# Performance work log

Hardware: AMD Instinct MI355X
Metric: run time of the kernel (lower is better)

## Reference

```python
import jax, jax.numpy as jnp
import numpy as np

N, E, D, H, C = 50000, 250000, 300, 4, 75  # nodes, edges, in_size=300, heads=4, out=75 (H*C=300)


def setup_inputs() -> dict:
    key = jax.random.key(0)
    ks = jax.random.split(key, 32)
    rn = lambda k, shape, s=0.05: jax.random.normal(k, shape, jnp.float32) * s
    inp = {}
    inp['x'] = rn(ks[0], (N, D), 1.0)
    inp['edge_index'] = jax.random.randint(ks[1], (2, E), 0, N, dtype=jnp.int32)
    inp['edge_attr'] = rn(ks[2], (E, 4), 1.0)
    inp['obj_normals'] = rn(ks[3], (N, 3), 1.0)
    # parameters (Linear stored as [in, out] so y = x @ W + b)
    inp['Wq'] = rn(ks[4], (D, H * C)); inp['bq'] = rn(ks[5], (H * C,))
    inp['Wk'] = rn(ks[6], (D, H * C)); inp['bk'] = rn(ks[7], (H * C,))
    inp['Wv'] = rn(ks[8], (D, H * C)); inp['bv'] = rn(ks[9], (H * C,))
    inp['We'] = rn(ks[10], (D, H * C))               # lin_edge, no bias
    inp['Wn'] = rn(ks[11], (3, D)); inp['bn'] = rn(ks[12], (D,))      # map_normal
    inp['Wxy'] = rn(ks[13], (2, D)); inp['bxy'] = rn(ks[14], (D,))    # map_xy_relative_coord
    inp['Wloc'] = rn(ks[15], (3 * D, D)); inp['bloc'] = rn(ks[16], (D,))  # map_back_edge_loc
    inp['Wobj'] = rn(ks[17], (2 * D, D)); inp['bobj'] = rn(ks[18], (D,))  # map_back_edge_obj
    inp['Wfus'] = rn(ks[19], (2 * D, D)); inp['bfus'] = rn(ks[20], (D,))  # hv_words_fusion
    inp['Wcls'] = rn(ks[21], (D, 5)); inp['bcls'] = rn(ks[22], (5,))      # horizontal_word_cls
    inp['Wskip'] = rn(ks[23], (D, H * C)); inp['bskip'] = rn(ks[24], (H * C,))  # lin_skip
    inp['vocab'] = rn(ks[25], (7, D), 1.0)  # spatial_vocab_we
    return inp


def reference(x, edge_index, edge_attr, obj_normals,
              Wq, bq, Wk, bk, Wv, bv, We, Wn, bn, Wxy, bxy,
              Wloc, bloc, Wobj, bobj, Wfus, bfus, Wcls, bcls,
              Wskip, bskip, vocab):
    src, dst = edge_index[0], edge_index[1]  # x_j = x[src], x_i = x[dst]
    x_i = x[dst]
    x_j = x[src]
    q = (x_i @ Wq + bq).reshape(E, H, C)
    k = (x_j @ Wk + bk).reshape(E, H, C)
    # vertical (top/bottom) word embeddings gated by edge_attr signs
    top = (edge_attr[:, 0] > 0).astype(x.dtype)[:, None] * vocab[0][None, :]
    bot = (edge_attr[:, 1] < 0).astype(x.dtype)[:, None] * vocab[1][None, :]
    vert = top + bot                                           # [E, D]
    # horizontal word probabilities from geometry + feature cues
    ni = obj_normals[dst] @ Wn + bn
    nj = obj_normals[src] @ Wn + bn
    xy = edge_attr[:, 2:4] @ Wxy + bxy
    loc = jnp.concatenate([xy, ni, nj], axis=1) @ Wloc + bloc
    obj = jnp.concatenate([x_i, x_j - x_i], axis=1) @ Wobj + bobj
    prob = jax.nn.softmax(jnp.tanh(obj + loc) @ Wcls + bcls, axis=1)   # [E, 5]
    horiz = prob @ vocab[2:7]                                  # [E, D]
    edge_word = jnp.concatenate([vert, horiz], axis=1) @ Wfus + bfus   # [E, D]
    ef = (edge_word @ We).reshape(E, H, C)                     # lin_edge
    k = k + ef
    # scaled dot-product attention with per-destination-node softmax
    alpha = (q * k).sum(-1) / jnp.asarray(np.sqrt(C), x.dtype)  # [E, H]
    m = jax.ops.segment_max(alpha, dst, num_segments=N)
    alpha = jnp.exp(alpha - m[dst])
    den = jax.ops.segment_sum(alpha, dst, num_segments=N)
    alpha = alpha / den[dst]
    v = (x_j @ Wv + bv).reshape(E, H, C) + ef
    msg = v * alpha[..., None]                                  # [E, H, C]
    out = jax.ops.segment_sum(msg, dst, num_segments=N).reshape(N, H * C)
    out = out + x @ Wskip + bskip                               # concat heads + root skip
    return out
```

## Files before the change

### kernel.cpp

```cpp
#include <hip/hip_runtime.h>
#include <hip/hip_bf16.h>
#include <math.h>

#define NDIM 300
#define KPAD 320
#define NREAL 1800
#define NPAD 1920

typedef __hip_bfloat16 bf16;
typedef __attribute__((ext_vector_type(8))) short short8;
typedef __attribute__((ext_vector_type(4))) float f32x4;

__device__ __forceinline__ void gl_lds16(const void* g, void* l) {
    __builtin_amdgcn_global_load_lds(
        (const __attribute__((address_space(1))) void*)g,
        (__attribute__((address_space(3))) void*)l, 16, 0, 0);
}

__device__ __forceinline__ float bflo(uint u) { return __uint_as_float(u << 16); }
__device__ __forceinline__ float bfhi(uint u) { return __uint_as_float(u & 0xFFFF0000u); }

__global__ void small_pre(
    const float* __restrict__ Wn, const float* __restrict__ bn,
    const float* __restrict__ Wxy, const float* __restrict__ bxy,
    const float* __restrict__ Wloc, const float* __restrict__ bloc,
    const float* __restrict__ bobj,
    const float* __restrict__ Wfus,
    const float* __restrict__ vocab,
    float* __restrict__ Wn1, float* __restrict__ Wn2,
    float* __restrict__ Mxy, float* __restrict__ bgeo,
    float* __restrict__ vf5, float* __restrict__ t0, float* __restrict__ t1)
{
    int i = blockIdx.x * blockDim.x + threadIdx.x;
    if (i < 900) {
        int r = i / 300, c = i % 300;
        float s = 0.f;
        for (int k = 0; k < 300; k++) s += Wn[r*300+k] * Wloc[(300+k)*300+c];
        Wn1[i] = s;
    } else if (i < 1800) {
        int j = i - 900; int r = j/300, c = j%300;
        float s = 0.f;
        for (int k = 0; k < 300; k++) s += Wn[r*300+k] * Wloc[(600+k)*300+c];
        Wn2[j] = s;
    } else if (i < 2400) {
        int j = i - 1800; int r = j/300, c = j%300;
        float s = 0.f;
        for (int k = 0; k < 300; k++) s += Wxy[r*300+k] * Wloc[k*300+c];
        Mxy[j] = 2.f * s;
    } else if (i < 2700) {
        int c = i - 2400;
        float s = bloc[c] + bobj[c];
        for (int k = 0; k < 300; k++) s += bxy[k] * Wloc[k*300+c];
        for (int k = 0; k < 300; k++) s += bn[k] * (Wloc[(300+k)*300+c] + Wloc[(600+k)*300+c]);
        bgeo[c] = 2.f * s;
    } else if (i < 4200) {
        int j = i - 2700; int p = j/300, c = j%300;
        float s = 0.f;
        for (int k = 0; k < 300; k++) s += vocab[(2+p)*300+k] * Wfus[(300+k)*300+c];
        vf5[j] = s;
    } else if (i < 4500) {
        int c = i - 4200;
        float s = 0.f;
        for (int k = 0; k < 300; k++) s += vocab[k] * Wfus[k*300+c];
        t0[c] = s;
    } else if (i < 4800) {
        int c = i - 4500;
        float s = 0.f;
        for (int k = 0; k < 300; k++) s += vocab[300+k] * Wfus[k*300+c];
        t1[c] = s;
    }
}

__global__ void small_pre2(
    const float* __restrict__ We, const float* __restrict__ bfus,
    const float* __restrict__ vf5, const float* __restrict__ t0, const float* __restrict__ t1,
    const float* __restrict__ Wcls,
    float* __restrict__ E8, float* __restrict__ WclsT)
{
    int i = blockIdx.x * blockDim.x + threadIdx.x;
    if (i < 2400) {
        int r = i / 300, c = i % 300;
        const float* src;
        if (r == 0) src = t0;
        else if (r == 1) src = t1;
        else if (r == 7) src = bfus;
        else src = vf5 + (r - 2) * 300;
        float s = 0.f;
        for (int k = 0; k < 300; k++) s += src[k] * We[k*300+c];
        E8[i] = s;
    } else if (i < 3900) {
        int j = i - 2400; int cl = j / 300, c = j % 300;
        WclsT[cl * 300 + c] = Wcls[c * 5 + cl];
    }
}

__global__ void pack_w(
    const float* __restrict__ Wq, const float* __restrict__ Wk,
    const float* __restrict__ Wv, const float* __restrict__ Wskip,
    const float* __restrict__ Wobj,
    const float* __restrict__ Wn1, const float* __restrict__ Wn2,
    const float* __restrict__ bq, const float* __restrict__ bk,
    const float* __restrict__ bv, const float* __restrict__ bskip,
    bf16* __restrict__ WcatT, float* __restrict__ bcat)
{
    int i = blockIdx.x * blockDim.x + threadIdx.x;
    if (i < NREAL) {
        int c = i;
        float b = 0.f;
        if (c < 600)       { if (!(c & 1)) b = bq[c >> 1]; }
        else if (c < 1200) { int cc = c - 600; if (cc & 1) b = bk[cc >> 1]; }
        else if (c < 1500) b = bv[c - 1200];
        else               b = bskip[c - 1500];
        bcat[i] = b;
    }
    if (i < NPAD * KPAD) {
        int cp = i / KPAD, k = i % KPAD;
        float v = 0.f;
        if (cp < NREAL) {
            int seg, jj;
            if (cp < 600)       { jj = cp >> 1; seg = (cp & 1) ? 4 : 0; }
            else if (cp < 1200) { int cc = cp - 600; jj = cc >> 1; seg = (cc & 1) ? 1 : 5; }
            else if (cp < 1500) { jj = cp - 1200; seg = 2; }
            else                { jj = cp - 1500; seg = 3; }
            if (k < 300) {
                switch (seg) {
                    case 0: v = Wq[k*300+jj]; break;
                    case 1: v = Wk[k*300+jj]; break;
                    case 2: v = Wv[k*300+jj]; break;
                    case 3: v = Wskip[k*300+jj]; break;
                    case 4: v = Wobj[k*300+jj] - Wobj[(300+k)*300+jj]; break;
                    default: v = Wobj[(300+k)*300+jj]; break;
                }
            } else if (k < 303) {
                if (seg == 4) v = Wn1[(k-300)*300+jj];
                else if (seg == 5) v = Wn2[(k-300)*300+jj];
            }
            if (seg >= 4) v *= 2.f;
        }
        WcatT[i] = __float2bfloat16(v);
    }
}

__global__ void conv_xb(const float* __restrict__ X, const float* __restrict__ Nrm,
                        bf16* __restrict__ Xb, int M)
{
    int i = blockIdx.x * blockDim.x + threadIdx.x;
    int row = i / 40, c8 = i % 40;
    if (row >= M) return;
    int c0 = c8 * 8;
    union { bf16 h[8]; short8 s; } u;
    #pragma unroll
    for (int t = 0; t < 8; t++) {
        int c = c0 + t;
        float v = 0.f;
        if (c < 300)      v = X[(size_t)row * 300 + c];
        else if (c < 303) v = Nrm[(size_t)row * 3 + (c - 300)];
        u.h[t] = __float2bfloat16(v);
    }
    *(short8*)&Xb[(size_t)row * 320 + c0] = u.s;
}

__global__ __launch_bounds__(256) void qe8_k(
    const bf16* __restrict__ QP, const float* __restrict__ E8,
    float* __restrict__ QE8f, int N)
{
    __shared__ unsigned short Qs[64 * 302];
    const int tid = threadIdx.x;
    const int n0 = blockIdx.x * 64;
    const int nrows = min(64, N - n0);
    const int nu = nrows * 300;
    const uint* src = (const uint*)QP + (size_t)n0 * 300;
    for (int i = tid; i < nu; i += 256) {
        int rr = i / 300, cc = i - rr * 300;
        Qs[rr * 302 + cc] = (unsigned short)src[i];
    }
    __syncthreads();
    const int w = tid >> 6, l = tid & 63;
    if (l >= nrows) return;
    float acc[8] = {0.f,0.f,0.f,0.f,0.f,0.f,0.f,0.f};
    const int cb = 75 * w;
    for (int cc = 0; cc < 75; cc++) {
        int c = cb + cc;
        float qv = __uint_as_float(((uint)Qs[l * 302 + c]) << 16);
        #pragma unroll
        for (int s = 0; s < 8; s++) acc[s] += qv * E8[s * 300 + c];
    }
    float* out = QE8f + (size_t)(n0 + l) * 32;
    #pragma unroll
    for (int s = 0; s < 8; s++) out[s * 4 + w] = acc[s];
}

__global__ void hist_k(const int* __restrict__ ei, int* __restrict__ deg, int E) {
    int e = blockIdx.x * blockDim.x + threadIdx.x;
    if (e < E) atomicAdd(&deg[ei[E + e]], 1);
}

__global__ __launch_bounds__(1024) void scan_local(
    const int* __restrict__ deg, int* __restrict__ off, int* __restrict__ bsum, int N)
{
    __shared__ int buf[1024];
    int i = blockIdx.x * 1024 + threadIdx.x;
    int v = (i < N) ? deg[i] : 0;
    buf[threadIdx.x] = v;
    __syncthreads();
    #pragma unroll
    for (int ofs = 1; ofs < 1024; ofs <<= 1) {
        int t = (threadIdx.x >= ofs) ? buf[threadIdx.x - ofs] : 0;
        __syncthreads();
        buf[threadIdx.x] += t;
        __syncthreads();
    }
    if (i < N) off[i] = buf[threadIdx.x] - v;
    if (threadIdx.x == 1023) bsum[blockIdx.x] = buf[1023];
}

__global__ __launch_bounds__(1024) void scan_bsum(
    const int* __restrict__ bsum, int* __restrict__ bexc, int nb)
{
    __shared__ int buf[1024];
    int v = (threadIdx.x < nb) ? bsum[threadIdx.x] : 0;
    buf[threadIdx.x] = v;
    __syncthreads();
    #pragma unroll
    for (int ofs = 1; ofs < 1024; ofs <<= 1) {
        int t = (threadIdx.x >= ofs) ? buf[threadIdx.x - ofs] : 0;
        __syncthreads();
        buf[threadIdx.x] += t;
        __syncthreads();
    }
    if (threadIdx.x < nb) bexc[threadIdx.x] = buf[threadIdx.x] - v;
}

__global__ void scan_add(int* __restrict__ off, int* __restrict__ cur,
                         const int* __restrict__ bexc, int N, int E)
{
    int i = blockIdx.x * blockDim.x + threadIdx.x;
    if (i < N) {
        int o = off[i] + bexc[i >> 10];
        off[i] = o; cur[i] = o;
    }
    if (i == 0) off[N] = E;
}

__global__ void scatter_k(const int* __restrict__ ei, const float* __restrict__ ea,
                          int* __restrict__ cur,
                          int2* __restrict__ esd, float* __restrict__ eas, int E) {
    int e = blockIdx.x * blockDim.x + threadIdx.x;
    if (e < E) {
        int s = ei[e];
        int d = ei[E + e];
        float4 a = *(const float4*)&ea[(size_t)e * 4];
        int p = atomicAdd(&cur[d], 1);
        esd[p] = make_int2(s, d);
        *(float4*)&eas[(size_t)p * 4] = a;
    }
}

__global__ __launch_bounds__(256) void gemm_mfma(
    const bf16* __restrict__ Xb,
    const bf16* __restrict__ Bt, const float* __restrict__ bcat,
    bf16* __restrict__ QP, bf16* __restrict__ PK, bf16* __restrict__ V,
    float* __restrict__ Ot, int M)
{
    __shared__ __align__(16) bf16 As[2][128 * 32];
    __shared__ __align__(16) bf16 Bs[2][128 * 32];

    const int tid  = threadIdx.x;
    const int wave = tid >> 6;
    const int lane = tid & 63;
    const int r0 = blockIdx.y * 128;
    const int c0 = blockIdx.x * 128;
    const int wm = (wave >> 1) * 64;
    const int wn = (wave & 1) * 64;
    const int lr = lane & 15;
    const int lq = lane >> 4;

    f32x4 acc[4][4];
    #pragma unroll
    for (int j = 0; j < 4; j++)
        #pragma unroll
        for (int i = 0; i < 4; i++) acc[j][i] = (f32x4){0.f, 0.f, 0.f, 0.f};

    const int bcol_l = lane >> 2;
    const int bkp    = (lane & 3) * 8;

    auto stage = [&](int buf, int kb) {
        #pragma unroll
        for (int h = 0; h < 2; h++) {
            int tbase = h * 256 + wave * 64;
            int t = tbase + lane;
            int grow = min(r0 + (t >> 2), M - 1);
            gl_lds16(Xb + (size_t)grow * 320 + kb + (t & 3) * 8,
                     &As[buf][tbase * 8]);
        }
        #pragma unroll
        for (int h = 0; h < 2; h++) {
            int cloc = wave * 32 + h * 16;
            gl_lds16(Bt + (size_t)(c0 + cloc + bcol_l) * KPAD + kb + bkp,
                     &Bs[buf][cloc * 32]);
        }
    };

    stage(0, 0);
    #pragma unroll
    for (int it = 0; it < 10; it++) {
        __syncthreads();
        if (it < 9) stage((it + 1) & 1, (it + 1) * 32);
        const int b = it & 1;
        short8 af[4], bfr[4];
        #pragma unroll
        for (int i = 0; i < 4; i++)
            af[i] = *(const short8*)&As[b][(wm + i * 16 + lr) * 32 + lq * 8];
        #pragma unroll
        for (int j = 0; j < 4; j++)
            bfr[j] = *(const short8*)&Bs[b][(wn + j * 16 + lr) * 32 + lq * 8];
        #pragma unroll
        for (int j = 0; j < 4; j++)
            #pragma unroll
            for (int i = 0; i < 4; i++)
                acc[j][i] = __builtin_amdgcn_mfma_f32_16x16x32_bf16(
                    bfr[j], af[i], acc[j][i], 0, 0, 0);
    }

    #pragma unroll
    for (int j = 0; j < 4; j++) {
        int colb = c0 + wn + j * 16 + lq * 4;
        if (colb >= NREAL) continue;
        float4 bb = *(const float4*)&bcat[colb];
        #pragma unroll
        for (int i = 0; i < 4; i++) {
            int row = r0 + wm + i * 16 + lr;
            if (row >= M) continue;
            float v0 = acc[j][i][0] + bb.x;
            float v1 = acc[j][i][1] + bb.y;
            float v2 = acc[j][i][2] + bb.z;
            float v3 = acc[j][i][3] + bb.w;
            if (colb < 1500) {
                union { bf16 h[4]; uint2 u2; } p;
                p.h[0] = __float2bfloat16(v0); p.h[1] = __float2bfloat16(v1);
                p.h[2] = __float2bfloat16(v2); p.h[3] = __float2bfloat16(v3);
                if (colb < 600)
                    *(uint2*)&QP[(size_t)row * 600 + colb] = p.u2;
                else if (colb < 1200)
                    *(uint2*)&PK[(size_t)row * 600 + (colb - 600)] = p.u2;
                else
                    *(uint2*)&V[(size_t)row * 300 + (colb - 1200)] = p.u2;
            } else {
                *(float4*)&Ot[(size_t)row * 300 + (colb - 1500)] =
                    make_float4(v0, v1, v2, v3);
            }
        }
    }
}

__global__ __launch_bounds__(256) void edge_alpha(
    const int2* __restrict__ esd, const float* __restrict__ eas,
    const bf16* __restrict__ QP, const bf16* __restrict__ PK,
    const float* __restrict__ Mxy, const float* __restrict__ bgeo,
    const float* __restrict__ QE8f, const float* __restrict__ WclsT,
    const float* __restrict__ bcls,
    float* __restrict__ AW,
    int E, int nwaves)
{
    __shared__ __align__(16) float red[4][20 * 68];
    __shared__ float res[4][20];
    const int wv   = threadIdx.x >> 6;
    const int lane = threadIdx.x & 63;
    float* __restrict__ rw = red[wv];
    float* __restrict__ rs = res[wv];
    const int gw  = blockIdx.x * 4 + wv;
    const int per = (E + nwaves - 1) / nwaves;
    const int t0  = gw * per;
    if (t0 >= E) return;
    const int t1 = min(t0 + per, E);
    const bool ok4 = lane < 44;

    float mx0[5], mx1[5], bg[5], wcl[5][5];
    #pragma unroll
    for (int r = 0; r < 4; r++) {
        int c = lane + 64 * r;
        mx0[r] = Mxy[c]; mx1[r] = Mxy[300 + c]; bg[r] = bgeo[c];
        #pragma unroll
        for (int cl = 0; cl < 5; cl++) wcl[cl][r] = WclsT[cl * 300 + c];
    }
    {
        int c = lane + 256;
        mx0[4] = ok4 ? Mxy[c] : 0.f;
        mx1[4] = ok4 ? Mxy[300 + c] : 0.f;
        bg[4]  = ok4 ? bgeo[c] : 0.f;
        #pragma unroll
        for (int cl = 0; cl < 5; cl++) wcl[cl][4] = ok4 ? WclsT[cl * 300 + c] : 0.f;
    }
    float bc[5];
    #pragma unroll
    for (int cl = 0; cl < 5; cl++) bc[cl] = bcls[cl];
    const float isc = 0.11547005383792516f;

    const uint* QPu = (const uint*)QP;
    const uint* PKu = (const uint*)PK;

    int prev_d = -1;
    float qv[5], pib[5];
    float prt[18];

    auto reload = [&](int dd) {
        const uint* qr = QPu + (size_t)dd * 300 + lane;
        #pragma unroll
        for (int r = 0; r < 4; r++) {
            uint uq = qr[64 * r];
            qv[r] = bflo(uq); pib[r] = bfhi(uq) + bg[r];
        }
        uint uq = ok4 ? qr[256] : 0u;
        qv[4] = bflo(uq); pib[4] = bfhi(uq) + bg[4];
    };
    auto compute = [&](const uint (&pk)[5], float az, float aw_, int ub) {
        float tt[5], qk[5];
        #pragma unroll
        for (int r = 0; r < 5; r++) {
            float pj = bflo(pk[r]), kf = bfhi(pk[r]);
            float v = pib[r] + pj + az * mx0[r] + aw_ * mx1[r];
            tt[r] = fmaf(-2.f, __builtin_amdgcn_rcpf(1.f + __expf(v)), 1.f);
            qk[r] = qv[r] * kf;
        }
        #pragma unroll
        for (int cl = 0; cl < 5; cl++)
            prt[ub + cl] = tt[0]*wcl[cl][0] + tt[1]*wcl[cl][1] + tt[2]*wcl[cl][2]
                         + tt[3]*wcl[cl][3] + tt[4]*wcl[cl][4];
        float h0 = qk[0], h3 = qk[4], h1 = 0.f, h2 = 0.f;
        if (lane < 11) h0 += qk[1]; else h1 += qk[1];
        if (lane < 22) h1 += qk[2]; else h2 += qk[2];
        if (lane < 33) h2 += qk[3]; else h3 += qk[3];
        prt[ub+5] = h0; prt[ub+6] = h1; prt[ub+7] = h2; prt[ub+8] = h3;
    };

    for (int t = t0; t < t1; t += 2) {
        const int i0 = t;
        const int i1 = (t + 1 < t1) ? t + 1 : t;
        const int2 sd0 = esd[i0], sd1 = esd[i1];
        const float4 a40 = *(const float4*)&eas[(size_t)4 * i0];
        const float4 a41 = *(const float4*)&eas[(size_t)4 * i1];

        uint pk0[5], pk1[5];
        const uint* p0r = PKu + (size_t)sd0.x * 300 + lane;
        const uint* p1r = PKu + (size_t)sd1.x * 300 + lane;
        #pragma unroll
        for (int r = 0; r < 4; r++) { pk0[r] = p0r[64 * r]; pk1[r] = p1r[64 * r]; }
        pk0[4] = ok4 ? p0r[256] : 0u;
        pk1[4] = ok4 ? p1r[256] : 0u;

        if (sd0.y != prev_d) reload(sd0.y);
        compute(pk0, a40.z, a40.w, 0);
        if (sd1.y != sd0.y) reload(sd1.y);
        compute(pk1, a41.z, a41.w, 9);
        prev_d = sd1.y;

        #pragma unroll
        for (int v = 0; v < 18; v++) rw[v * 68 + lane] = prt[v];
        #pragma unroll
        for (int i = 0; i < 5; i++) {
            int v = 4 * i + (lane >> 4);
            const f32x4 q4 = *(const f32x4*)&rw[v * 68 + (lane & 15) * 4];
            float s = (q4[0] + q4[1]) + (q4[2] + q4[3]);
            s += __shfl_xor(s, 1, 64);
            s += __shfl_xor(s, 2, 64);
            s += __shfl_xor(s, 4, 64);
            s += __shfl_xor(s, 8, 64);
            if ((lane & 15) == 0 && v < 18) rs[v] = s;
        }
        {
            const int    u  = lane >> 5;
            const int    ub = u * 9;
            const float4 au = u ? a41 : a40;
            const int    dd = u ? sd1.y : sd0.y;
            const int    tw = u ? i1 : i0;
            float lg0 = rs[ub+0] + bc[0], lg1 = rs[ub+1] + bc[1], lg2 = rs[ub+2] + bc[2];
            float lg3 = rs[ub+3] + bc[3], lg4 = rs[ub+4] + bc[4];
            float mxv = fmaxf(fmaxf(fmaxf(lg0, lg1), fmaxf(lg2, lg3)), lg4);
            float p0 = __expf(lg0 - mxv), p1 = __expf(lg1 - mxv), p2 = __expf(lg2 - mxv);
            float p3 = __expf(lg3 - mxv), p4 = __expf(lg4 - mxv);
            float pinv = __builtin_amdgcn_rcpf(p0 + p1 + p2 + p3 + p4);
            p0 *= pinv; p1 *= pinv; p2 *= pinv; p3 *= pinv; p4 *= pinv;
            float ct  = au.x > 0.f ? 1.f : 0.f;
            float cb_ = au.y < 0.f ? 1.f : 0.f;
            const f32x4* qe = (const f32x4*)(QE8f + (size_t)dd * 32);
            f32x4 addv = ct*qe[0] + cb_*qe[1] + p0*qe[2] + p1*qe[3]
                       + p2*qe[4] + p3*qe[5] + p4*qe[6] + qe[7];
            float ax0 = __expf((rs[ub+5] + addv[0]) * isc);
            float ax1 = __expf((rs[ub+6] + addv[1]) * isc);
            float ax2 = __expf((rs[ub+7] + addv[2]) * isc);
            float ax3 = __expf((rs[ub+8] + addv[3]) * isc);
            if ((lane & 31) == 0) {
                float* awp = AW + (size_t)12 * tw;
                *(float4*)(awp)     = make_float4(ax0, ax1, ax2, ax3);
                *(float4*)(awp + 4) = make_float4(ct, cb_, p0, p1);
                *(float4*)(awp + 8) = make_float4(p2, p3, p4, 0.f);
            }
        }
    }
}

__global__ __launch_bounds__(256) void node_pv(
    const int2* __restrict__ esd, const bf16* __restrict__ V,
    const float* __restrict__ E8, const float* __restrict__ AW,
    const int* __restrict__ off,
    float* __restrict__ Ot, int N)
{
    const int wid  = threadIdx.x >> 6;
    const int lane = threadIdx.x & 63;
    const int n = blockIdx.x * 4 + wid;
    if (n >= N) return;
    const int e0 = off[n], e1 = off[n + 1];
    if (e0 == e1) return;
    const size_t nrow = (size_t)n * 300;
    const bool ok4 = lane < 44;

    float e8r[8][5];
    #pragma unroll
    for (int rr = 0; rr < 8; rr++) {
        #pragma unroll
        for (int r = 0; r < 4; r++) e8r[rr][r] = E8[rr * 300 + lane + 64 * r];
        e8r[rr][4] = ok4 ? E8[rr * 300 + lane + 256] : 0.f;
    }

    float macc[5] = {0.f, 0.f, 0.f, 0.f, 0.f};
    float den0 = 0.f, den1 = 0.f, den2 = 0.f, den3 = 0.f;

    auto body = [&](int t) {
        int s = esd[t].x;
        const float* awp = AW + (size_t)12 * t;
        float4 ax = *(const float4*)(awp);
        float4 wa = *(const float4*)(awp + 4);
        float4 wb = *(const float4*)(awp + 8);
        const bf16* vr = V + (size_t)s * 300 + lane;
        #pragma unroll
        for (int r = 0; r < 5; r++) {
            float vv = (r < 4) ? __bfloat162float(vr[64 * r])
                               : (ok4 ? __bfloat162float(vr[256]) : 0.f);
            float efc = wa.x * e8r[0][r] + wa.y * e8r[1][r] + wa.z * e8r[2][r] + wa.w * e8r[3][r]
                      + wb.x * e8r[4][r] + wb.y * e8r[5][r] + wb.z * e8r[6][r] + e8r[7][r];
            float w = (r == 0) ? ax.x
                    : (r == 1) ? (lane < 11 ? ax.x : ax.y)
                    : (r == 2) ? (lane < 22 ? ax.y : ax.z)
                    : (r == 3) ? (lane < 33 ? ax.z : ax.w)
                    : ax.w;
            macc[r] += w * (vv + efc);
        }
        den0 += ax.x; den1 += ax.y; den2 += ax.z; den3 += ax.w;
    };
    int t = e0;
    for (; t + 1 < e1; t += 2) { body(t); body(t + 1); }
    if (t < e1) body(t);

    const float rd0 = __builtin_amdgcn_rcpf(den0);
    const float rd1 = __builtin_amdgcn_rcpf(den1);
    const float rd2 = __builtin_amdgcn_rcpf(den2);
    const float rd3 = __builtin_amdgcn_rcpf(den3);
    #pragma unroll
    for (int r = 0; r < 5; r++) {
        int c = lane + 64 * r;
        if (c < 300) {
            float rd = (r == 0) ? rd0
                     : (r == 1) ? (lane < 11 ? rd0 : rd1)
                     : (r == 2) ? (lane < 22 ? rd1 : rd2)
                     : (r == 3) ? (lane < 33 ? rd2 : rd3)
                     : rd3;
            Ot[nrow + c] += macc[r] * rd;
        }
    }
}

extern "C" void kernel_launch(void* const* d_in, const int* in_sizes, int n_in,
                              void* d_out, int out_size, void* d_ws, size_t ws_size,
                              hipStream_t stream)
{
    const float* x     = (const float*)d_in[0];
    const int*   ei    = (const int*)  d_in[1];
    const float* ea    = (const float*)d_in[2];
    const float* on    = (const float*)d_in[3];
    const float* Wq    = (const float*)d_in[4];
    const float* bq    = (const float*)d_in[5];
    const float* Wk    = (const float*)d_in[6];
    const float* bk    = (const float*)d_in[7];
    const float* Wv    = (const float*)d_in[8];
    const float* bv    = (const float*)d_in[9];
    const float* We    = (const float*)d_in[10];
    const float* Wn    = (const float*)d_in[11];
    const float* bn    = (const float*)d_in[12];
    const float* Wxy   = (const float*)d_in[13];
    const float* bxy   = (const float*)d_in[14];
    const float* Wloc  = (const float*)d_in[15];
    const float* bloc  = (const float*)d_in[16];
    const float* Wobj  = (const float*)d_in[17];
    const float* bobj  = (const float*)d_in[18];
    const float* Wfus  = (const float*)d_in[19];
    const float* bfus  = (const float*)d_in[20];
    const float* Wcls  = (const float*)d_in[21];
    const float* bcls  = (const float*)d_in[22];
    const float* Wskip = (const float*)d_in[23];
    const float* bskip = (const float*)d_in[24];
    const float* vocab = (const float*)d_in[25];

    const int N = in_sizes[0] / NDIM;
    const int E = in_sizes[1] / 2;

    const size_t nodeElems = (size_t)N * 300;
    const size_t wcatElems = (size_t)NPAD * KPAD;
    const size_t xbElems   = (size_t)N * 320;
    size_t xbBytes = xbElems * sizeof(bf16);
    const size_t ovlBytes = ((size_t)16 * E + (size_t)32 * N) * sizeof(float);
    if (ovlBytes > xbBytes) xbBytes = ovlBytes;

    const size_t f32Elems  = NREAL + 904 + 904 + 600 + 304 + 1504 + 304 + 304 + 2400 + 1504;
    const size_t intElems  = (size_t)N + (size_t)(N + 1) + (size_t)N
                           + (size_t)2 * E + 2048;
    size_t need = (5 * nodeElems + wcatElems) * sizeof(bf16) + xbBytes
                + f32Elems * sizeof(float) + intElems * sizeof(int);
    if (ws_size < need) return;

    bf16* wsh = (bf16*)d_ws;
    bf16* QPb   = wsh;
    bf16* PKb   = QPb + (size_t)2 * nodeElems;
    bf16* Vb    = PKb + (size_t)2 * nodeElems;
    bf16* WcatT = Vb + nodeElems;
    bf16* Xb    = WcatT + wcatElems;
    float* AW   = (float*)Xb;
    float* eas  = AW + (size_t)12 * E;
    float* QE8f = eas + (size_t)4 * E;
    float* ws = (float*)((char*)Xb + xbBytes);
    size_t o = 0;
    float* bcat  = ws + o; o += NREAL;
    float* Wn1   = ws + o; o += 904;
    float* Wn2   = ws + o; o += 904;
    float* Mxyb  = ws + o; o += 600;
    float* bgeo  = ws + o; o += 304;
    float* vf5   = ws + o; o += 1504;
    float* t0b   = ws + o; o += 304;
    float* t1b   = ws + o; o += 304;
    float* E8b   = ws + o; o += 2400;
    float* WclsT = ws + o; o += 1504;
    int* ip = (int*)(ws + o);
    int* deg    = ip;             ip += N;
    int* offb   = ip;             ip += N + 1;
    int* curb   = ip;             ip += N;
    int2* esd   = (int2*)ip;      ip += (size_t)2 * E;
    int* bsum   = ip;             ip += 1024;
    int* bexc   = ip;             ip += 1024;
    (void)n_in; (void)out_size;

    hipMemsetAsync(deg, 0, (size_t)N * sizeof(int), stream);

    small_pre<<<19, 256, 0, stream>>>(Wn, bn, Wxy, bxy, Wloc, bloc, bobj, Wfus, vocab,
                                      Wn1, Wn2, Mxyb, bgeo, vf5, t0b, t1b);
    small_pre2<<<16, 256, 0, stream>>>(We, bfus, vf5, t0b, t1b, Wcls, E8b, WclsT);
    pack_w<<<(NPAD * KPAD + 255) / 256, 256, 0, stream>>>(
        Wq, Wk, Wv, Wskip, Wobj, Wn1, Wn2, bq, bk, bv, bskip, WcatT, bcat);
    conv_xb<<<((size_t)N * 40 + 255) / 256, 256, 0, stream>>>(x, on, Xb, N);

    const int ebk = (E + 255) / 256;
    hist_k<<<ebk, 256, 0, stream>>>(ei, deg, E);
    const int nbl = (N + 1023) / 1024;
    scan_local<<<nbl, 1024, 0, stream>>>(deg, offb, bsum, N);
    scan_bsum<<<1, 1024, 0, stream>>>(bsum, bexc, nbl);
    scan_add<<<(N + 255) / 256, 256, 0, stream>>>(offb, curb, bexc, N, E);

    dim3 g1(NPAD / 128, (N + 127) / 128);
    gemm_mfma<<<g1, 256, 0, stream>>>(Xb, WcatT, bcat,
                                      QPb, PKb, Vb, (float*)d_out, N);

    scatter_k<<<ebk, 256, 0, stream>>>(ei, ea, curb, esd, eas, E);
    qe8_k<<<(N + 63) / 64, 256, 0, stream>>>(QPb, E8b, QE8f, N);

    const int eab = 2048;
    edge_alpha<<<eab, 256, 0, stream>>>(esd, eas, QPb, PKb,
                                        Mxyb, bgeo, QE8f, WclsT, bcls,
                                        AW, E, eab * 4);

    const int nb = (N + 3) / 4;
    node_pv<<<nb, 256, 0, stream>>>(esd, Vb, E8b, AW,
                                    offb, (float*)d_out, N);
}
```

Baseline: 674.9 us.

## Stage GEMM epilogue through LDS for coalesced stores and swizzle block order

The GEMM epilogue now writes accumulators into shared memory and then stores rows contiguously, so global writes to QP/PK/V and the fp32 output are coalesced instead of scattered 8- or 16-byte fragments. The launch grid is also flattened to 1D and remapped so that groups of 8 row panels sweep across all 15 column tiles, which is meant to improve L2 reuse of the X tiles. In exchange the epilogue gains extra syncthreads and LDS round trips, and the fp32 tail tile is written in two halves.

Measured after the change: 637.2 us. 5.6% less time.

```diff
diff --git a/kernel.cpp b/kernel.cpp
--- a/kernel.cpp
+++ b/kernel.cpp
@@ -260,16 +260,33 @@
     const bf16* __restrict__ Xb,
     const bf16* __restrict__ Bt, const float* __restrict__ bcat,
     bf16* __restrict__ QP, bf16* __restrict__ PK, bf16* __restrict__ V,
-    float* __restrict__ Ot, int M)
-{
-    __shared__ __align__(16) bf16 As[2][128 * 32];
-    __shared__ __align__(16) bf16 Bs[2][128 * 32];
+    float* __restrict__ Ot, int M, int npan)
+{
+    __shared__ __align__(16) char smraw[34816];
+    bf16*  Asb = (bf16*)smraw;
+    bf16*  Bsb = (bf16*)(smraw + 16384);
+    bf16*  EP  = (bf16*)smraw;
+    float* EPf = (float*)smraw;
+
+    const int bid = blockIdx.x;
+    int p, cx;
+    {
+        const int full = (npan >> 3) * 120;
+        if (bid < full) {
+            int g = bid / 120, r = bid - g * 120;
+            p = (g << 3) + (r & 7); cx = r >> 3;
+        } else {
+            int r = bid - full;
+            int tp = npan & 7;
+            p = (npan & ~7) + r % tp; cx = r / tp;
+        }
+    }
+    const int r0 = p * 128;
+    const int c0 = cx * 128;
 
     const int tid  = threadIdx.x;
     const int wave = tid >> 6;
     const int lane = tid & 63;
-    const int r0 = blockIdx.y * 128;
-    const int c0 = blockIdx.x * 128;
     const int wm = (wave >> 1) * 64;
     const int wn = (wave & 1) * 64;
     const int lr = lane & 15;
@@ -291,13 +308,13 @@
             int t = tbase + lane;
             int grow = min(r0 + (t >> 2), M - 1);
             gl_lds16(Xb + (size_t)grow * 320 + kb + (t & 3) * 8,
-                     &As[buf][tbase * 8]);
+                     &Asb[buf * 4096 + tbase * 8]);
         }
         #pragma unroll
         for (int h = 0; h < 2; h++) {
             int cloc = wave * 32 + h * 16;
             gl_lds16(Bt + (size_t)(c0 + cloc + bcol_l) * KPAD + kb + bkp,
-                     &Bs[buf][cloc * 32]);
+                     &Bsb[buf * 4096 + cloc * 32]);
         }
     };
 
@@ -310,10 +327,10 @@
         short8 af[4], bfr[4];
         #pragma unroll
         for (int i = 0; i < 4; i++)
-            af[i] = *(const short8*)&As[b][(wm + i * 16 + lr) * 32 + lq * 8];
+            af[i] = *(const short8*)&Asb[b * 4096 + (wm + i * 16 + lr) * 32 + lq * 8];
         #pragma unroll
         for (int j = 0; j < 4; j++)
-            bfr[j] = *(const short8*)&Bs[b][(wn + j * 16 + lr) * 32 + lq * 8];
+            bfr[j] = *(const short8*)&Bsb[b * 4096 + (wn + j * 16 + lr) * 32 + lq * 8];
         #pragma unroll
         for (int j = 0; j < 4; j++)
             #pragma unroll
@@ -322,32 +339,70 @@
                     bfr[j], af[i], acc[j][i], 0, 0, 0);
     }
 
-    #pragma unroll
-    for (int j = 0; j < 4; j++) {
-        int colb = c0 + wn + j * 16 + lq * 4;
-        if (colb >= NREAL) continue;
-        float4 bb = *(const float4*)&bcat[colb];
-        #pragma unroll
-        for (int i = 0; i < 4; i++) {
-            int row = r0 + wm + i * 16 + lr;
-            if (row >= M) continue;
-            float v0 = acc[j][i][0] + bb.x;
-            float v1 = acc[j][i][1] + bb.y;
-            float v2 = acc[j][i][2] + bb.z;
-            float v3 = acc[j][i][3] + bb.w;
-            if (colb < 1500) {
-                union { bf16 h[4]; uint2 u2; } p;
-                p.h[0] = __float2bfloat16(v0); p.h[1] = __float2bfloat16(v1);
-                p.h[2] = __float2bfloat16(v2); p.h[3] = __float2bfloat16(v3);
-                if (colb < 600)
-                    *(uint2*)&QP[(size_t)row * 600 + colb] = p.u2;
-                else if (colb < 1200)
-                    *(uint2*)&PK[(size_t)row * 600 + (colb - 600)] = p.u2;
-                else
-                    *(uint2*)&V[(size_t)row * 300 + (colb - 1200)] = p.u2;
-            } else {
-                *(float4*)&Ot[(size_t)row * 300 + (colb - 1500)] =
-                    make_float4(v0, v1, v2, v3);
+    __syncthreads();
+
+    if (c0 < 1500) {
+        #pragma unroll
+        for (int j = 0; j < 4; j++) {
+            int colL = wn + j * 16 + lq * 4;
+            float4 bb = *(const float4*)&bcat[c0 + colL];
+            #pragma unroll
+            for (int i = 0; i < 4; i++) {
+                int row = wm + i * 16 + lr;
+                union { bf16 h[4]; uint2 u2; } pk;
+                pk.h[0] = __float2bfloat16(acc[j][i][0] + bb.x);
+                pk.h[1] = __float2bfloat16(acc[j][i][1] + bb.y);
+                pk.h[2] = __float2bfloat16(acc[j][i][2] + bb.z);
+                pk.h[3] = __float2bfloat16(acc[j][i][3] + bb.w);
+                *(uint2*)&EP[row * 136 + colL] = pk.u2;
+            }
+        }
+        __syncthreads();
+        #pragma unroll
+        for (int rep = 0; rep < 32; rep++) {
+            int row = rep * 4 + wave;
+            int gr = r0 + row;
+            int col = c0 + 2 * lane;
+            if (gr < M && col < 1500) {
+                uint val = *(const uint*)&EP[row * 136 + 2 * lane];
+                if (col < 600)       *(uint*)&QP[(size_t)gr * 600 + col] = val;
+                else if (col < 1200) *(uint*)&PK[(size_t)gr * 600 + (col - 600)] = val;
+                else                 *(uint*)&V [(size_t)gr * 300 + (col - 1200)] = val;
+            }
+        }
+    }
+    if (c0 + 128 > 1500) {
+        #pragma unroll
+        for (int h = 0; h < 2; h++) {
+            __syncthreads();
+            if ((wave & 1) == h) {
+                #pragma unroll
+                for (int j = 0; j < 4; j++) {
+                    int colL = j * 16 + lq * 4;
+                    int colb = c0 + h * 64 + colL;
+                    if (colb < NREAL) {
+                        float4 bb = *(const float4*)&bcat[colb];
+                        #pragma unroll
+                        for (int i = 0; i < 4; i++) {
+                            int row = wm + i * 16 + lr;
+                            f32x4 vv;
+                            vv[0] = acc[j][i][0] + bb.x;
+                            vv[1] = acc[j][i][1] + bb.y;
+                            vv[2] = acc[j][i][2] + bb.z;
+                            vv[3] = acc[j][i][3] + bb.w;
+                            *(f32x4*)&EPf[row * 68 + colL] = vv;
+                        }
+                    }
+                }
+            }
+            __syncthreads();
+            #pragma unroll
+            for (int rep = 0; rep < 32; rep++) {
+                int row = rep * 4 + wave;
+                int gr = r0 + row;
+                int col = c0 + h * 64 + lane;
+                if (gr < M && col >= 1500 && col < NREAL)
+                    Ot[(size_t)gr * 300 + (col - 1500)] = EPf[row * 68 + lane];
             }
         }
     }
@@ -663,9 +718,9 @@
     scan_bsum<<<1, 1024, 0, stream>>>(bsum, bexc, nbl);
     scan_add<<<(N + 255) / 256, 256, 0, stream>>>(offb, curb, bexc, N, E);
 
-    dim3 g1(NPAD / 128, (N + 127) / 128);
-    gemm_mfma<<<g1, 256, 0, stream>>>(Xb, WcatT, bcat,
-                                      QPb, PKb, Vb, (float*)d_out, N);
+    const int npan = (N + 127) / 128;
+    gemm_mfma<<<npan * 15, 256, 0, stream>>>(Xb, WcatT, bcat,
+                                             QPb, PKb, Vb, (float*)d_out, N, npan);
 
     scatter_k<<<ebk, 256, 0, stream>>>(ei, ea, curb, esd, eas, E);
     qe8_k<<<(N + 63) / 64, 256, 0, stream>>>(QPb, E8b, QE8f, N);
```
